# Optimization experiments

Measured on AMD Instinct MI355X. Metric: run time of the kernel, lower is better.

The kernel has to match this reference:

```python
import jax, jax.numpy as jnp
import numpy as np

HIDDEN = 128

def setup_inputs() -> dict:
    key = jax.random.key(0)
    ks = jax.random.split(key, 7)
    B, T, I, O = 256, 512, 256, 1000
    s_ih = 1.0 / np.sqrt(HIDDEN)
    x = jax.random.normal(ks[0], (B, T, I), dtype=jnp.float32)
    W_ih = jax.random.uniform(ks[1], (HIDDEN, I), minval=-s_ih, maxval=s_ih, dtype=jnp.float32)
    W_hh = jax.random.uniform(ks[2], (HIDDEN, HIDDEN), minval=-s_ih, maxval=s_ih, dtype=jnp.float32)
    b_ih = jax.random.uniform(ks[3], (HIDDEN,), minval=-s_ih, maxval=s_ih, dtype=jnp.float32)
    b_hh = jax.random.uniform(ks[4], (HIDDEN,), minval=-s_ih, maxval=s_ih, dtype=jnp.float32)
    s_fc = 1.0 / np.sqrt(HIDDEN)
    W_fc = jax.random.uniform(ks[5], (O, HIDDEN), minval=-s_fc, maxval=s_fc, dtype=jnp.float32)
    b_fc = jax.random.uniform(ks[6], (O,), minval=-s_fc, maxval=s_fc, dtype=jnp.float32)
    return {"x": x, "W_ih": W_ih, "W_hh": W_hh, "b_ih": b_ih, "b_hh": b_hh, "W_fc": W_fc, "b_fc": b_fc}


def reference(x, W_ih, W_hh, b_ih, b_hh, W_fc, b_fc):
    B = x.shape[0]
    # Precompute input projection for all timesteps in one big GEMM: [B,T,H]
    xp = jnp.einsum('bti,hi->bth', x, W_ih) + b_ih + b_hh
    h0 = jnp.zeros((B, HIDDEN), dtype=x.dtype)

    def step(h, xp_t):
        h = jnp.tanh(xp_t + h @ W_hh.T)
        return h, None

    # scan over time axis; only the final hidden state feeds the fc head
    h_last, _ = jax.lax.scan(step, h0, jnp.swapaxes(xp, 0, 1))
    return h_last @ W_fc.T + b_fc
```

## Files before the change

kernel.cpp:

```cpp
#include <hip/hip_runtime.h>


#define HID    128
#define TSTEPS 512
#define BATCH  256
#define INDIM  256
#define ODIM   1000

typedef _Float16 f16x8 __attribute__((ext_vector_type(8)));
typedef __fp16   fp16x2 __attribute__((ext_vector_type(2)));
typedef float    f32x4 __attribute__((ext_vector_type(4)));

__device__ __forceinline__ unsigned pk16(float a, float b) {
    union { fp16x2 h; unsigned u; } t;
    t.h = __builtin_amdgcn_cvt_pkrtz(a, b);
    return t.u;
}
__device__ __forceinline__ float tanh_fast(float v) {
    float e = __expf(2.f * v);
    float r = __builtin_amdgcn_rcpf(e + 1.f);
    return __builtin_fmaf(-2.f, r, 1.f);
}

__global__ __launch_bounds__(256) void k_phase1(const float* __restrict__ x,
                                                const float* __restrict__ Wih,
                                                const float* __restrict__ bih,
                                                const float* __restrict__ bhh,
                                                float* __restrict__ xp) {
    __shared__ __align__(16) _Float16 xs[2][4096];
    __shared__ __align__(16) _Float16 wsm[2][4096];

    const int tid  = threadIdx.x;
    const int wave = tid >> 6, lane = tid & 63;
    const int quad = lane >> 4, l16 = lane & 15;
    const int wm = wave >> 1, wn = wave & 1;
    const int m0 = blockIdx.x * 128;

    int srow[4], scol[4], sdst[4];
#pragma unroll
    for (int q = 0; q < 4; q++) {
        int li = q * 256 + tid;
        srow[q] = li >> 3;
        scol[q] = li & 7;
        sdst[q] = srow[q] * 32 + ((((scol[q] >> 1) ^ srow[q]) & 3) << 3) + ((scol[q] & 1) << 2);
    }

    float bias_v[4];
#pragma unroll
    for (int nt = 0; nt < 4; nt++) {
        int j = wn * 64 + nt * 16 + l16;
        bias_v[nt] = bih[j] + bhh[j];
    }

    float4 rx[4], rw[4];
#define LOAD_STAGE(KC)                                                              \
    {                                                                               \
        _Pragma("unroll") for (int q = 0; q < 4; q++) {                             \
            rx[q] = *(const float4*)(x + (size_t)(m0 + srow[q]) * INDIM + (KC) * 32 + scol[q] * 4); \
            rw[q] = *(const float4*)(Wih + (size_t)srow[q] * INDIM + (KC) * 32 + scol[q] * 4);      \
        }                                                                           \
    }
#define WRITE_STAGE(BUF)                                                            \
    {                                                                               \
        _Pragma("unroll") for (int q = 0; q < 4; q++) {                             \
            uint2 px, pw;                                                           \
            px.x = pk16(rx[q].x, rx[q].y); px.y = pk16(rx[q].z, rx[q].w);           \
            pw.x = pk16(rw[q].x, rw[q].y); pw.y = pk16(rw[q].z, rw[q].w);           \
            *(uint2*)&xs[BUF][sdst[q]]  = px;                                       \
            *(uint2*)&wsm[BUF][sdst[q]] = pw;                                       \
        }                                                                           \
    }

    f32x4 acc[4][4];
#pragma unroll
    for (int mt = 0; mt < 4; mt++)
#pragma unroll
        for (int nt = 0; nt < 4; nt++) {
            acc[mt][nt].x = 0.f; acc[mt][nt].y = 0.f;
            acc[mt][nt].z = 0.f; acc[mt][nt].w = 0.f;
        }

    LOAD_STAGE(0);
    WRITE_STAGE(0);
    __syncthreads();

    for (int kc = 0; kc < 8; kc++) {
        const int b = kc & 1;
        if (kc < 7) LOAD_STAGE(kc + 1);

        f16x8 a[4], bw[4];
#pragma unroll
        for (int mt = 0; mt < 4; mt++) {
            int row = wm * 64 + mt * 16 + l16;
            a[mt] = *(const f16x8*)&xs[b][row * 32 + (((quad ^ row) & 3) << 3)];
        }
#pragma unroll
        for (int nt = 0; nt < 4; nt++) {
            int row = wn * 64 + nt * 16 + l16;
            bw[nt] = *(const f16x8*)&wsm[b][row * 32 + (((quad ^ row) & 3) << 3)];
        }
#pragma unroll
        for (int mt = 0; mt < 4; mt++)
#pragma unroll
            for (int nt = 0; nt < 4; nt++)
                acc[mt][nt] = __builtin_amdgcn_mfma_f32_16x16x32_f16(a[mt], bw[nt], acc[mt][nt], 0, 0, 0);

        if (kc < 7) WRITE_STAGE(b ^ 1);
        __syncthreads();
    }

#pragma unroll
    for (int mt = 0; mt < 4; mt++)
#pragma unroll
        for (int nt = 0; nt < 4; nt++)
#pragma unroll
            for (int reg = 0; reg < 4; reg++) {
                int row = m0 + wm * 64 + mt * 16 + quad * 4 + reg;
                xp[(size_t)row * HID + wn * 64 + nt * 16 + l16] = acc[mt][nt][reg] + bias_v[nt];
            }
#undef LOAD_STAGE
#undef WRITE_STAGE
}

#define RNN_STEP4(TV, XQI, XQC, PB) {                                             \
    _Pragma("unroll") for (int reg = 0; reg < 4; reg++) {                         \
        float hv = tanh_fast(C[reg]);                                             \
        int m = quad * 4 + reg;                                                   \
        hp[PB][m * 128 + ((((jbase >> 3) ^ m) & 15) << 3) + (jbase & 7)] =        \
            (_Float16)hv;                                                         \
    }                                                                             \
    if ((TV) + 4 < TSTEPS) {                                                      \
        _Pragma("unroll") for (int reg = 0; reg < 4; reg++)                       \
            XQI[reg] = xpb[ib[reg] + ((TV) + 4) * HID];                           \
    }                                                                             \
    __syncthreads();                                                              \
    f16x8 A[4];                                                                   \
    _Pragma("unroll") for (int kc = 0; kc < 4; kc++)                              \
        A[kc] = *(const f16x8*)&hp[PB][l16 * 128 + ((((kc * 4 + quad) ^ l16) & 15) << 3)]; \
    f32x4 ch, cl;                                                                 \
    ch.x = XQC[0]; ch.y = XQC[1]; ch.z = XQC[2]; ch.w = XQC[3];                   \
    cl.x = 0.f; cl.y = 0.f; cl.z = 0.f; cl.w = 0.f;                               \
    ch = __builtin_amdgcn_mfma_f32_16x16x32_f16(A[0], Bf[0], ch, 0, 0, 0);        \
    cl = __builtin_amdgcn_mfma_f32_16x16x32_f16(A[2], Bf[2], cl, 0, 0, 0);        \
    ch = __builtin_amdgcn_mfma_f32_16x16x32_f16(A[1], Bf[1], ch, 0, 0, 0);        \
    cl = __builtin_amdgcn_mfma_f32_16x16x32_f16(A[3], Bf[3], cl, 0, 0, 0);        \
    C = ch + cl;                                                                  \
}

__global__ __launch_bounds__(512) void k_rnn4(const float* __restrict__ Whh,
                                              float* __restrict__ ws) {
    __shared__ __align__(16) _Float16 hp[2][16 * 128];
    const int tid  = threadIdx.x;
    const int wave = tid >> 6, lane = tid & 63;
    const int quad = lane >> 4, l16 = lane & 15;
    const int r0    = blockIdx.x * 16;
    const int jbase = wave * 16 + l16;

    f16x8 Bf[4];
#pragma unroll
    for (int kc = 0; kc < 4; kc++) {
        const float* p = Whh + (size_t)jbase * HID + kc * 32 + quad * 8;
        float4 e0 = *(const float4*)p, e1 = *(const float4*)(p + 4);
        union { unsigned u[4]; f16x8 v; } t;
        t.u[0] = pk16(e0.x, e0.y); t.u[1] = pk16(e0.z, e0.w);
        t.u[2] = pk16(e1.x, e1.y); t.u[3] = pk16(e1.z, e1.w);
        Bf[kc] = t.v;
    }

    const float* xpb = ws;
    int ib[4];
#pragma unroll
    for (int reg = 0; reg < 4; reg++)
        ib[reg] = (r0 + quad * 4 + reg) * (TSTEPS * HID) + jbase;

    f32x4 C;
    float xq0[4], xq1[4], xq2[4], xq3[4];
    C.x = xpb[ib[0]]; C.y = xpb[ib[1]]; C.z = xpb[ib[2]]; C.w = xpb[ib[3]];
#pragma unroll
    for (int reg = 0; reg < 4; reg++) {
        xq1[reg] = xpb[ib[reg] + 1 * HID];
        xq2[reg] = xpb[ib[reg] + 2 * HID];
        xq3[reg] = xpb[ib[reg] + 3 * HID];
    }

    for (int t = 0; t < 508; t += 4) {
        RNN_STEP4(t,     xq0, xq1, 0);
        RNN_STEP4(t + 1, xq1, xq2, 1);
        RNN_STEP4(t + 2, xq2, xq3, 0);
        RNN_STEP4(t + 3, xq3, xq0, 1);
    }
    RNN_STEP4(508, xq0, xq1, 0);
    RNN_STEP4(509, xq1, xq2, 1);
    RNN_STEP4(510, xq2, xq3, 0);

#pragma unroll
    for (int reg = 0; reg < 4; reg++)
        ws[ib[reg]] = tanh_fast(C[reg]);
}

__global__ __launch_bounds__(256) void k_fc(const float* __restrict__ ws,
                                            const float* __restrict__ Wfc,
                                            const float* __restrict__ bfc,
                                            float* __restrict__ out) {
    __shared__ float hb[HID];
    const int b   = blockIdx.x;
    const int tid = threadIdx.x;
    if (tid < HID) hb[tid] = ws[(size_t)b * (TSTEPS * HID) + tid];
    __syncthreads();

    for (int o = tid; o < ODIM; o += 256) {
        const float* wr = Wfc + (size_t)o * HID;
        float acc = 0.f;
#pragma unroll
        for (int q = 0; q < 32; q++) {
            float4 wv = *(const float4*)(wr + q * 4);
            float4 hv = *(const float4*)&hb[q * 4];
            acc += wv.x * hv.x + wv.y * hv.y + wv.z * hv.z + wv.w * hv.w;
        }
        out[(size_t)b * ODIM + o] = acc + bfc[o];
    }
}

extern "C" void kernel_launch(void* const* d_in, const int* in_sizes, int n_in,
                              void* d_out, int out_size, void* d_ws, size_t ws_size,
                              hipStream_t stream) {
    const float* x   = (const float*)d_in[0];
    const float* Wih = (const float*)d_in[1];
    const float* Whh = (const float*)d_in[2];
    const float* bih = (const float*)d_in[3];
    const float* bhh = (const float*)d_in[4];
    const float* Wfc = (const float*)d_in[5];
    const float* bfc = (const float*)d_in[6];
    float* out = (float*)d_out;
    float* ws  = (float*)d_ws;

    k_phase1<<<dim3(1024), dim3(256), 0, stream>>>(x, Wih, bih, bhh, ws);
    k_rnn4  <<<dim3(16),   dim3(512), 0, stream>>>(Whh, ws);
    k_fc    <<<dim3(BATCH), dim3(256), 0, stream>>>(ws, Wfc, bfc, out);
}
```

Measured before the change: 393.7 us.

## Restructure RNN recurrence kernel to 4 waves with transposed MFMA and vector loads

The recurrence kernel drops from 8 waves to 4 per block. Each wave now computes 32 hidden units via two MFMA tiles, with W_hh as the A operand and h as the B operand. This transposed layout lets each lane load contiguous f32x4 input projections and write packed fp16 hidden values as 8-byte stores, instead of scalar strided loads and 2-byte stores. A raw s_waitcnt plus s_barrier replaces __syncthreads. The aim is to cut per-step barrier cost across fewer waves and reduce LDS and global instruction counts on the latency-bound serial chain, at the cost of more MFMAs per wave per step.

```diff
diff --git a/kernel.cpp b/kernel.cpp
--- a/kernel.cpp
+++ b/kernel.cpp
@@ -122,81 +122,93 @@
 #undef WRITE_STAGE
 }
 
-#define RNN_STEP4(TV, XQI, XQC, PB) {                                             \
-    _Pragma("unroll") for (int reg = 0; reg < 4; reg++) {                         \
-        float hv = tanh_fast(C[reg]);                                             \
-        int m = quad * 4 + reg;                                                   \
-        hp[PB][m * 128 + ((((jbase >> 3) ^ m) & 15) << 3) + (jbase & 7)] =        \
-            (_Float16)hv;                                                         \
+#define RSTEP(TV, XI0, XI1, XC0, XC1, PB) {                                       \
+    uint2 pw0, pw1;                                                               \
+    pw0.x = pk16(tanh_fast(C0.x), tanh_fast(C0.y));                               \
+    pw0.y = pk16(tanh_fast(C0.z), tanh_fast(C0.w));                               \
+    pw1.x = pk16(tanh_fast(C1.x), tanh_fast(C1.y));                               \
+    pw1.y = pk16(tanh_fast(C1.z), tanh_fast(C1.w));                               \
+    *(uint2*)&hp[PB][waddr0] = pw0;                                               \
+    *(uint2*)&hp[PB][waddr1] = pw1;                                               \
+    if ((TV) + 4 < TSTEPS) {                                                      \
+        XI0 = *(const f32x4*)(xpb + ((TV) + 4) * HID);                            \
+        XI1 = *(const f32x4*)(xpb + ((TV) + 4) * HID + 16);                       \
     }                                                                             \
-    if ((TV) + 4 < TSTEPS) {                                                      \
-        _Pragma("unroll") for (int reg = 0; reg < 4; reg++)                       \
-            XQI[reg] = xpb[ib[reg] + ((TV) + 4) * HID];                           \
-    }                                                                             \
-    __syncthreads();                                                              \
-    f16x8 A[4];                                                                   \
-    _Pragma("unroll") for (int kc = 0; kc < 4; kc++)                              \
-        A[kc] = *(const f16x8*)&hp[PB][l16 * 128 + ((((kc * 4 + quad) ^ l16) & 15) << 3)]; \
-    f32x4 ch, cl;                                                                 \
-    ch.x = XQC[0]; ch.y = XQC[1]; ch.z = XQC[2]; ch.w = XQC[3];                   \
-    cl.x = 0.f; cl.y = 0.f; cl.z = 0.f; cl.w = 0.f;                               \
-    ch = __builtin_amdgcn_mfma_f32_16x16x32_f16(A[0], Bf[0], ch, 0, 0, 0);        \
-    cl = __builtin_amdgcn_mfma_f32_16x16x32_f16(A[2], Bf[2], cl, 0, 0, 0);        \
-    ch = __builtin_amdgcn_mfma_f32_16x16x32_f16(A[1], Bf[1], ch, 0, 0, 0);        \
-    cl = __builtin_amdgcn_mfma_f32_16x16x32_f16(A[3], Bf[3], cl, 0, 0, 0);        \
-    C = ch + cl;                                                                  \
-}
-
-__global__ __launch_bounds__(512) void k_rnn4(const float* __restrict__ Whh,
-                                              float* __restrict__ ws) {
+    asm volatile("s_waitcnt lgkmcnt(0)\n\ts_barrier" ::: "memory");               \
+    f16x8 hB0 = *(const f16x8*)&hp[PB][raddr0];                                   \
+    f16x8 hB1 = *(const f16x8*)&hp[PB][raddr1];                                   \
+    f16x8 hB2 = *(const f16x8*)&hp[PB][raddr2];                                   \
+    f16x8 hB3 = *(const f16x8*)&hp[PB][raddr3];                                   \
+    f32x4 c0h = XC0, c1h = XC1, c0l, c1l;                                         \
+    c0l.x = 0.f; c0l.y = 0.f; c0l.z = 0.f; c0l.w = 0.f;                           \
+    c1l.x = 0.f; c1l.y = 0.f; c1l.z = 0.f; c1l.w = 0.f;                           \
+    c0h = __builtin_amdgcn_mfma_f32_16x16x32_f16(Wf[0][0], hB0, c0h, 0, 0, 0);    \
+    c1h = __builtin_amdgcn_mfma_f32_16x16x32_f16(Wf[1][0], hB0, c1h, 0, 0, 0);    \
+    c0l = __builtin_amdgcn_mfma_f32_16x16x32_f16(Wf[0][2], hB2, c0l, 0, 0, 0);    \
+    c1l = __builtin_amdgcn_mfma_f32_16x16x32_f16(Wf[1][2], hB2, c1l, 0, 0, 0);    \
+    c0h = __builtin_amdgcn_mfma_f32_16x16x32_f16(Wf[0][1], hB1, c0h, 0, 0, 0);    \
+    c1h = __builtin_amdgcn_mfma_f32_16x16x32_f16(Wf[1][1], hB1, c1h, 0, 0, 0);    \
+    c0l = __builtin_amdgcn_mfma_f32_16x16x32_f16(Wf[0][3], hB3, c0l, 0, 0, 0);    \
+    c1l = __builtin_amdgcn_mfma_f32_16x16x32_f16(Wf[1][3], hB3, c1l, 0, 0, 0);    \
+    C0 = c0h + c0l; C1 = c1h + c1l;                                               \
+}
+
+__global__ __launch_bounds__(256) void k_rnn(const float* __restrict__ Whh,
+                                             float* __restrict__ ws) {
     __shared__ __align__(16) _Float16 hp[2][16 * 128];
     const int tid  = threadIdx.x;
     const int wave = tid >> 6, lane = tid & 63;
     const int quad = lane >> 4, l16 = lane & 15;
-    const int r0    = blockIdx.x * 16;
-    const int jbase = wave * 16 + l16;
-
-    f16x8 Bf[4];
-#pragma unroll
-    for (int kc = 0; kc < 4; kc++) {
-        const float* p = Whh + (size_t)jbase * HID + kc * 32 + quad * 8;
-        float4 e0 = *(const float4*)p, e1 = *(const float4*)(p + 4);
-        union { unsigned u[4]; f16x8 v; } t;
-        t.u[0] = pk16(e0.x, e0.y); t.u[1] = pk16(e0.z, e0.w);
-        t.u[2] = pk16(e1.x, e1.y); t.u[3] = pk16(e1.z, e1.w);
-        Bf[kc] = t.v;
-    }
-
-    const float* xpb = ws;
-    int ib[4];
-#pragma unroll
-    for (int reg = 0; reg < 4; reg++)
-        ib[reg] = (r0 + quad * 4 + reg) * (TSTEPS * HID) + jbase;
-
-    f32x4 C;
-    float xq0[4], xq1[4], xq2[4], xq3[4];
-    C.x = xpb[ib[0]]; C.y = xpb[ib[1]]; C.z = xpb[ib[2]]; C.w = xpb[ib[3]];
-#pragma unroll
-    for (int reg = 0; reg < 4; reg++) {
-        xq1[reg] = xpb[ib[reg] + 1 * HID];
-        xq2[reg] = xpb[ib[reg] + 2 * HID];
-        xq3[reg] = xpb[ib[reg] + 3 * HID];
-    }
+    const int row  = blockIdx.x * 16 + l16;
+
+    f16x8 Wf[2][4];
+#pragma unroll
+    for (int jt = 0; jt < 2; jt++)
+#pragma unroll
+        for (int kc = 0; kc < 4; kc++) {
+            const float* p = Whh + (size_t)(32 * wave + 16 * jt + l16) * HID + kc * 32 + quad * 8;
+            float4 e0 = *(const float4*)p, e1 = *(const float4*)(p + 4);
+            union { unsigned u[4]; f16x8 v; } t;
+            t.u[0] = pk16(e0.x, e0.y); t.u[1] = pk16(e0.z, e0.w);
+            t.u[2] = pk16(e1.x, e1.y); t.u[3] = pk16(e1.z, e1.w);
+            Wf[jt][kc] = t.v;
+        }
+
+    const int raddr0 = l16 * 128 + ((((0 * 4 + quad) ^ l16) & 15) << 3);
+    const int raddr1 = l16 * 128 + ((((1 * 4 + quad) ^ l16) & 15) << 3);
+    const int raddr2 = l16 * 128 + ((((2 * 4 + quad) ^ l16) & 15) << 3);
+    const int raddr3 = l16 * 128 + ((((3 * 4 + quad) ^ l16) & 15) << 3);
+    const int waddr0 = l16 * 128 + ((((4 * wave + 0 + (quad >> 1)) ^ l16) & 15) << 3) + ((quad & 1) << 2);
+    const int waddr1 = l16 * 128 + ((((4 * wave + 2 + (quad >> 1)) ^ l16) & 15) << 3) + ((quad & 1) << 2);
+
+    const float* xpb = ws + (size_t)row * (TSTEPS * HID) + 32 * wave + quad * 4;
+
+    f32x4 C0, C1, xa0, xa1, xb0, xb1, xc0, xc1, xd0, xd1;
+    C0  = *(const f32x4*)(xpb);
+    C1  = *(const f32x4*)(xpb + 16);
+    xb0 = *(const f32x4*)(xpb + 1 * HID); xb1 = *(const f32x4*)(xpb + 1 * HID + 16);
+    xc0 = *(const f32x4*)(xpb + 2 * HID); xc1 = *(const f32x4*)(xpb + 2 * HID + 16);
+    xd0 = *(const f32x4*)(xpb + 3 * HID); xd1 = *(const f32x4*)(xpb + 3 * HID + 16);
 
     for (int t = 0; t < 508; t += 4) {
-        RNN_STEP4(t,     xq0, xq1, 0);
-        RNN_STEP4(t + 1, xq1, xq2, 1);
-        RNN_STEP4(t + 2, xq2, xq3, 0);
-        RNN_STEP4(t + 3, xq3, xq0, 1);
-    }
-    RNN_STEP4(508, xq0, xq1, 0);
-    RNN_STEP4(509, xq1, xq2, 1);
-    RNN_STEP4(510, xq2, xq3, 0);
-
-#pragma unroll
-    for (int reg = 0; reg < 4; reg++)
-        ws[ib[reg]] = tanh_fast(C[reg]);
-}
+        RSTEP(t,     xa0, xa1, xb0, xb1, 0);
+        RSTEP(t + 1, xb0, xb1, xc0, xc1, 1);
+        RSTEP(t + 2, xc0, xc1, xd0, xd1, 0);
+        RSTEP(t + 3, xd0, xd1, xa0, xa1, 1);
+    }
+    RSTEP(508, xa0, xa1, xb0, xb1, 0);
+    RSTEP(509, xb0, xb1, xc0, xc1, 1);
+    RSTEP(510, xc0, xc1, xd0, xd1, 0);
+
+    f32x4 o0, o1;
+    o0.x = tanh_fast(C0.x); o0.y = tanh_fast(C0.y);
+    o0.z = tanh_fast(C0.z); o0.w = tanh_fast(C0.w);
+    o1.x = tanh_fast(C1.x); o1.y = tanh_fast(C1.y);
+    o1.z = tanh_fast(C1.z); o1.w = tanh_fast(C1.w);
+    *(f32x4*)(ws + (size_t)row * (TSTEPS * HID) + 32 * wave + quad * 4)      = o0;
+    *(f32x4*)(ws + (size_t)row * (TSTEPS * HID) + 32 * wave + 16 + quad * 4) = o1;
+}
+#undef RSTEP
 
 __global__ __launch_bounds__(256) void k_fc(const float* __restrict__ ws,
                                             const float* __restrict__ Wfc,
@@ -235,6 +247,6 @@
     float* ws  = (float*)d_ws;
 
     k_phase1<<<dim3(1024), dim3(256), 0, stream>>>(x, Wih, bih, bhh, ws);
-    k_rnn4  <<<dim3(16),   dim3(512), 0, stream>>>(Whh, ws);
+    k_rnn   <<<dim3(16),   dim3(256), 0, stream>>>(Whh, ws);
     k_fc    <<<dim3(BATCH), dim3(256), 0, stream>>>(ws, Wfc, bfc, out);
 }
```

New measurement: 423.3 us. +7.5%, slower.
